# Kernel tuning notes

Hardware: AMD Instinct MI355X
Metric: run time of the kernel (lower is better)

The kernel has to match this reference:

```python
import jax, jax.numpy as jnp
import numpy as np

N = 50000      # nodes
E = 1600000    # edges (before self loops)
B = 512        # graphs
D = 128        # gcn dim (constant across the 3 GAT layers)
H = 1024       # hidden_dim
O = 128        # output_dim
NEG_SLOPE = 0.2


def setup_inputs() -> dict:
    key = jax.random.key(0)
    ks = jax.random.split(key, 24)
    inp = {
        "x": jax.random.normal(ks[0], (N, D), jnp.float32),
        "edge_index": jax.random.randint(ks[1], (2, E), 0, N, dtype=jnp.int64),
        "edge_weight": jax.random.uniform(ks[2], (E,), jnp.float32),
        "batch": jnp.sort(jax.random.randint(ks[3], (N,), 0, B, dtype=jnp.int64)),
    }
    s = 1.0 / np.sqrt(D)
    for i in range(3):
        k = 4 + 4 * i
        inp[f"W{i+1}"] = jax.random.normal(ks[k], (D, D), jnp.float32) * s
        inp[f"as{i+1}"] = jax.random.normal(ks[k + 1], (D,), jnp.float32) * s
        inp[f"ad{i+1}"] = jax.random.normal(ks[k + 2], (D,), jnp.float32) * s
        inp[f"b{i+1}"] = jnp.zeros((D,), jnp.float32)
    inp["Wf1"] = jax.random.normal(ks[16], (D, H), jnp.float32) * s
    inp["bf1"] = jnp.zeros((H,), jnp.float32)
    inp["Wf2"] = jax.random.normal(ks[17], (H, O), jnp.float32) * (1.0 / np.sqrt(H))
    inp["bf2"] = jnp.zeros((O,), jnp.float32)
    return inp


def gat_conv(x, src, dst, W, a_src, a_dst, b):
    """PyG GATConv, heads=1: gather -> leakyrelu -> segment softmax -> scatter-add."""
    h = x @ W                                   # [N, D]
    e = jax.nn.leaky_relu(jnp.take(h @ a_src, src) + jnp.take(h @ a_dst, dst), NEG_SLOPE)  # [E']
    m = jax.ops.segment_max(e, dst, num_segments=N)
    ex = jnp.exp(e - m[dst])
    denom = jax.ops.segment_sum(ex, dst, num_segments=N)
    alpha = ex / denom[dst]                      # segment softmax over incoming edges
    out = jax.ops.segment_sum(alpha[:, None] * h[src], dst, num_segments=N)
    return out + b


def reference(x, edge_index, edge_weight, batch,
              W1, as1, ad1, b1, W2, as2, ad2, b2, W3, as3, ad3, b3,
              Wf1, bf1, Wf2, bf2):
    # GATConv adds self loops; edge_weight is unused by GATConv (faithful to original)
    loop = jnp.arange(N, dtype=edge_index.dtype)
    src = jnp.concatenate([edge_index[0], loop])
    dst = jnp.concatenate([edge_index[1], loop])

    h = gat_conv(x, src, dst, W1, as1, ad1, b1)
    h = jax.nn.relu(gat_conv(h, src, dst, W2, as2, ad2, b2))
    h = jax.nn.relu(gat_conv(h, src, dst, W3, as3, ad3, b3))

    # global mean pool (gep)
    sums = jax.ops.segment_sum(h, batch, num_segments=B)        # [B, D]
    counts = jax.ops.segment_sum(jnp.ones((N,), h.dtype), batch, num_segments=B)
    pooled = sums / jnp.maximum(counts, 1.0)[:, None]

    # MLP head; dropout is identity at inference
    o = jax.nn.relu(pooled) @ Wf1 + bf1
    o = jax.nn.relu(o) @ Wf2 + bf2
    return o
```

## Files before the change

### kernel.cpp

```cpp
#include <hip/hip_runtime.h>
#include <cstdint>
#include <cstddef>

#define NEG_SLOPE 0.2f

typedef _Float16 f16x8 __attribute__((ext_vector_type(8)));
typedef float f32x4v __attribute__((ext_vector_type(4)));

__device__ __forceinline__ unsigned enc_f(float f) {
  unsigned u = __float_as_uint(f);
  return (u & 0x80000000u) ? ~u : (u | 0x80000000u);
}
__device__ __forceinline__ float dec_f(unsigned u) {
  return (u & 0x80000000u) ? __uint_as_float(u ^ 0x80000000u) : __uint_as_float(~u);
}

#define AST 136
#define ABYTES (64 * AST * 2)
#define SMEM_BYTES (ABYTES + 4 * 64 * 2 * 4)

__global__ void k_bounds_prep(const int* __restrict__ batch, int N, int B,
                              int* __restrict__ gstart, unsigned* __restrict__ maxPart,
                              int* __restrict__ counts,
                              const float* __restrict__ W1, const float* __restrict__ W2,
                              const float* __restrict__ W3,
                              _Float16* __restrict__ Wt1, _Float16* __restrict__ Wt2,
                              _Float16* __restrict__ Wt3, int nbb) {
  int b = blockIdx.x;
  if (b >= nbb) {
    int wi = b - nbb;
    const float* W = (wi == 0) ? W1 : (wi == 1) ? W2 : W3;
    _Float16* Wt = (wi == 0) ? Wt1 : (wi == 1) ? Wt2 : Wt3;
    for (int i = threadIdx.x; i < 2048; i += 256) {
      int k = i >> 4, n8 = (i & 15) << 3;
      float4 v0 = *(const float4*)&W[(size_t)k * 128 + n8];
      float4 v1 = *(const float4*)&W[(size_t)k * 128 + n8 + 4];
      Wt[(size_t)(n8 + 0) * 128 + k] = (_Float16)v0.x;
      Wt[(size_t)(n8 + 1) * 128 + k] = (_Float16)v0.y;
      Wt[(size_t)(n8 + 2) * 128 + k] = (_Float16)v0.z;
      Wt[(size_t)(n8 + 3) * 128 + k] = (_Float16)v0.w;
      Wt[(size_t)(n8 + 4) * 128 + k] = (_Float16)v1.x;
      Wt[(size_t)(n8 + 5) * 128 + k] = (_Float16)v1.y;
      Wt[(size_t)(n8 + 6) * 128 + k] = (_Float16)v1.z;
      Wt[(size_t)(n8 + 7) * 128 + k] = (_Float16)v1.w;
    }
    return;
  }
  int n = b * blockDim.x + threadIdx.x;
  if (n < 768) maxPart[n] = 0u;
  if (n >= N) return;
  counts[n] = 0;
  int cur = batch[n];
  if (n == 0) {
    for (int g = 0; g <= cur; g++) gstart[g] = 0;
  } else {
    int prev = batch[n - 1];
    for (int g = prev + 1; g <= cur; g++) gstart[g] = n;
  }
  if (n == N - 1) {
    for (int g = cur + 1; g <= B; g++) gstart[g] = N;
  }
}

__global__ void k_count_rank(const int* __restrict__ dst, int e0, int e1,
                             int* counts, int* __restrict__ rank) {
  int e = e0 + blockIdx.x * blockDim.x + threadIdx.x;
  if (e < e1) rank[e] = atomicAdd(&counts[dst[e]], 1);
}

__global__ __launch_bounds__(1024) void k_scan1(const int* __restrict__ counts, int N,
                                                int* __restrict__ row_ptr, int* __restrict__ part) {
  __shared__ int tmp[1024];
  int t = threadIdx.x;
  int i = blockIdx.x * 1024 + t;
  int v = (i < N) ? 1 + counts[i] : 0;
  tmp[t] = v;
  __syncthreads();
  for (int off = 1; off < 1024; off <<= 1) {
    int u = (t >= off) ? tmp[t - off] : 0;
    __syncthreads();
    tmp[t] += u;
    __syncthreads();
  }
  if (i < N) row_ptr[i + 1] = tmp[t];
  if (t == 1023) part[blockIdx.x] = tmp[t];
}

__global__ __launch_bounds__(1024) void k_scan3(int* __restrict__ row_ptr,
                                                const int* __restrict__ part, int N) {
  __shared__ int s_off;
  int bi = blockIdx.x;
  if (threadIdx.x == 0) {
    int run = 0;
    for (int b = 0; b < bi; b++) run += part[b];
    s_off = run;
    if (bi == 0) row_ptr[0] = 0;
  }
  __syncthreads();
  int i = bi * 1024 + threadIdx.x;
  if (i < N) row_ptr[i + 1] += s_off;
}

__device__ __forceinline__ void gemm_body(char* smem, int bx,
                                          const float* __restrict__ A32,
                                          const unsigned short* __restrict__ A16,
                                          const _Float16* __restrict__ WtG,
                                          unsigned short* __restrict__ hb,
                                          const float* __restrict__ asrc,
                                          const float* __restrict__ adst,
                                          float* __restrict__ sv, float* __restrict__ dv,
                                          unsigned* __restrict__ maxSlot, int M) {
  _Float16* Ah = (_Float16*)smem;
  float (*sred)[64][2] = (float (*)[64][2])(smem + ABYTES);
  int t = threadIdx.x;
  int rowbase = bx * 64;

  if (A16) {
    for (int i = t; i < 64 * 16; i += 256) {
      int r = i >> 4, c8 = (i & 15) << 3;
      int gr = rowbase + r;
      uint4 v = make_uint4(0u, 0u, 0u, 0u);
      if (gr < M) v = *(const uint4*)&A16[(size_t)gr * 128 + c8];
      *(uint4*)&Ah[r * AST + c8] = v;
    }
  } else {
    for (int i = t; i < 64 * 32; i += 256) {
      int r = i >> 5, c4 = (i & 31) << 2;
      int gr = rowbase + r;
      float4 v = make_float4(0.f, 0.f, 0.f, 0.f);
      if (gr < M) v = *(const float4*)&A32[(size_t)gr * 128 + c4];
      _Float16 tmp[4] = {(_Float16)v.x, (_Float16)v.y, (_Float16)v.z, (_Float16)v.w};
      *(short4*)&Ah[r * AST + c4] = *(short4*)tmp;
    }
  }
  __syncthreads();

  int wave = t >> 6, lane = t & 63, quad = lane >> 4, l15 = lane & 15;
  f32x4v acc[4][2];
#pragma unroll
  for (int mt = 0; mt < 4; mt++)
#pragma unroll
    for (int nt = 0; nt < 2; nt++) {
      acc[mt][nt][0] = 0.f; acc[mt][nt][1] = 0.f; acc[mt][nt][2] = 0.f; acc[mt][nt][3] = 0.f;
    }

#pragma unroll
  for (int s = 0; s < 4; s++) {
    int k0 = (s << 5) + (quad << 3);
    f16x8 af[4], bf[2];
#pragma unroll
    for (int mt = 0; mt < 4; mt++)
      af[mt] = *(f16x8*)&Ah[(mt * 16 + l15) * AST + k0];
#pragma unroll
    for (int nt = 0; nt < 2; nt++)
      bf[nt] = *(const f16x8*)&WtG[(size_t)(wave * 32 + nt * 16 + l15) * 128 + k0];
#pragma unroll
    for (int mt = 0; mt < 4; mt++)
#pragma unroll
      for (int nt = 0; nt < 2; nt++)
        acc[mt][nt] = __builtin_amdgcn_mfma_f32_16x16x32_f16(af[mt], bf[nt], acc[mt][nt], 0, 0, 0);
  }
  __syncthreads();

  float avv0 = asrc[wave * 32 + l15],      avv1 = asrc[wave * 32 + 16 + l15];
  float adv0 = adst[wave * 32 + l15],      adv1 = adst[wave * 32 + 16 + l15];
  _Float16* hS16 = (_Float16*)smem;
#pragma unroll
  for (int mt = 0; mt < 4; mt++) {
#pragma unroll
    for (int rr = 0; rr < 4; rr++) {
      int row = mt * 16 + quad * 4 + rr;
      hS16[row * AST + wave * 32 + l15]      = (_Float16)acc[mt][0][rr];
      hS16[row * AST + wave * 32 + 16 + l15] = (_Float16)acc[mt][1][rr];
      float ps = acc[mt][0][rr] * avv0 + acc[mt][1][rr] * avv1;
      float pd = acc[mt][0][rr] * adv0 + acc[mt][1][rr] * adv1;
#pragma unroll
      for (int mask = 8; mask; mask >>= 1) {
        ps += __shfl_xor(ps, mask);
        pd += __shfl_xor(pd, mask);
      }
      if (l15 == 0) { sred[wave][row][0] = ps; sred[wave][row][1] = pd; }
    }
  }
  __syncthreads();

  int tx = t & 31, ty = t >> 5;
#pragma unroll
  for (int r8 = 0; r8 < 8; r8++) {
    int row = r8 * 8 + ty;
    int gr = rowbase + row;
    if (gr < M)
      *(uint2*)&hb[(size_t)gr * 128 + tx * 4] = *(const uint2*)&hS16[row * AST + tx * 4];
  }

  if (t < 64) {
    int gr = rowbase + t;
    float ps = sred[0][t][0] + sred[1][t][0] + sred[2][t][0] + sred[3][t][0];
    float pd = sred[0][t][1] + sred[1][t][1] + sred[2][t][1] + sred[3][t][1];
    float wmax = -1e30f;
    if (gr < M) { sv[gr] = ps; dv[gr] = pd; wmax = ps; }
#pragma unroll
    for (int mask = 32; mask; mask >>= 1) wmax = fmaxf(wmax, __shfl_xor(wmax, mask));
    if (t == 0) atomicMax(&maxSlot[bx & 255], enc_f(wmax));
  }
}

__global__ __launch_bounds__(256) void k_fill_gemm(const int* __restrict__ src,
                                                   const int* __restrict__ dst,
                                                   const int* __restrict__ rank, int E, int N,
                                                   const int* __restrict__ row_ptr,
                                                   int* __restrict__ col,
                                                   const float* __restrict__ A32,
                                                   const _Float16* __restrict__ WtG,
                                                   unsigned short* __restrict__ hb,
                                                   const float* __restrict__ asrc,
                                                   const float* __restrict__ adst,
                                                   float* __restrict__ sv, float* __restrict__ dv,
                                                   unsigned* __restrict__ maxSlot, int Gg) {
  __shared__ __align__(16) char smem[SMEM_BYTES];
  int b = (int)blockIdx.x;
  bool isGemm = ((b % 9) == 4) && ((b / 9) < Gg);
  if (isGemm) {
    gemm_body(smem, b / 9, A32, (const unsigned short*)nullptr, WtG,
              hb, asrc, adst, sv, dv, maxSlot, N);
  } else {
    int nGemmBefore = (b >= 4) ? min((b - 4) / 9 + 1, Gg) : 0;
    int i = (b - nGemmBefore) * 256 + threadIdx.x;
    if (i < N) col[row_ptr[i]] = i;
    int e = i - N;
    if (e >= 0 && e < E) col[row_ptr[dst[e]] + 1 + rank[e]] = src[e];
  }
}

__global__ __launch_bounds__(256) void k_gemm_fused(const unsigned short* __restrict__ A16,
                                                    const _Float16* __restrict__ WtG,
                                                    unsigned short* __restrict__ hb,
                                                    const float* __restrict__ asrc,
                                                    const float* __restrict__ adst,
                                                    float* __restrict__ sv, float* __restrict__ dv,
                                                    unsigned* __restrict__ maxSlot, int M) {
  __shared__ __align__(16) char smem[SMEM_BYTES];
  gemm_body(smem, (int)blockIdx.x, (const float*)nullptr, A16, WtG,
            hb, asrc, adst, sv, dv, maxSlot, M);
}

__global__ __launch_bounds__(256) void k_agg(const unsigned short* __restrict__ hb,
                                             const float* __restrict__ sv,
                                             const float* __restrict__ dv,
                                             const int* __restrict__ row_ptr,
                                             const int* __restrict__ col,
                                             const float* __restrict__ bias,
                                             const unsigned* __restrict__ maxSlot,
                                             unsigned short* __restrict__ out16,
                                             int N, int relu) {
  int wid = (int)((blockIdx.x * (size_t)blockDim.x + threadIdx.x) >> 6);
  int lane = threadIdx.x & 63;
  if (wid >= N) return;

  unsigned mp = max(max(maxSlot[lane], maxSlot[lane + 64]),
                    max(maxSlot[lane + 128], maxSlot[lane + 192]));
#pragma unroll
  for (int off = 32; off; off >>= 1) mp = max(mp, __shfl_xor(mp, off));
  float maxS = dec_f(mp);

  int beg = row_ptr[wid], end = row_ptr[wid + 1];
  float dn = dv[wid];
  float m = maxS + dn;
  m = (m > 0.f) ? m : NEG_SLOPE * m;

  int g = lane >> 4, sub = lane & 15;
  const uint32_t* hbu = (const uint32_t*)hb;
  float acc[8];
#pragma unroll
  for (int k = 0; k < 8; k++) acc[k] = 0.f;
  float dsum = 0.f;

#define FETCH_SLOT(K, W, H)                                                \
  {                                                                        \
    int sl = ((K) << 2) + g;                                               \
    int sn = __shfl(sn_l, sl);                                             \
    W = __shfl(w_l, sl);                                                   \
    H = make_uint4(0u, 0u, 0u, 0u);                                        \
    if (sl < cnt) H = *(const uint4*)(hbu + (size_t)sn * 64 + sub * 4);    \
  }
#define ACC_SLOT(W, H)                                                     \
  {                                                                        \
    const _Float16* hp = (const _Float16*)&H;                              \
    _Pragma("unroll")                                                      \
    for (int q = 0; q < 8; q++) acc[q] += W * (float)hp[q];                \
  }

  for (int base = beg; base < end; base += 64) {
    int cnt = min(end - base, 64);

    int sn_l = 0;
    float w_l = 0.f;
    if (lane < cnt) {
      sn_l = col[base + lane];
      float e = sv[sn_l] + dn;
      e = (e > 0.f) ? e : NEG_SLOPE * e;
      w_l = __expf(e - m);
      dsum += w_l;
    }

    int kmaxW = (cnt + 3) >> 2;
    float wA, wB, wC, wD, wE, wF;
    uint4 hA, hB, hC, hD, hE, hF;
    FETCH_SLOT(0, wA, hA);
    FETCH_SLOT(1, wB, hB);
    FETCH_SLOT(2, wC, hC);
    FETCH_SLOT(3, wD, hD);
    FETCH_SLOT(4, wE, hE);
    for (int k = 5; k < kmaxW; k++) {
      FETCH_SLOT(k, wF, hF);
      ACC_SLOT(wA, hA);
      wA = wB; hA = hB;
      wB = wC; hB = hC;
      wC = wD; hC = hD;
      wD = wE; hD = hE;
      wE = wF; hE = hF;
    }
    ACC_SLOT(wA, hA);
    ACC_SLOT(wB, hB);
    ACC_SLOT(wC, hC);
    ACC_SLOT(wD, hD);
    ACC_SLOT(wE, hE);
  }

#pragma unroll
  for (int off = 1; off < 64; off <<= 1) dsum += __shfl_xor(dsum, off);
#pragma unroll
  for (int k = 0; k < 8; k++) {
    acc[k] += __shfl_xor(acc[k], 16);
    acc[k] += __shfl_xor(acc[k], 32);
  }
  if (lane < 16) {
    float inv = 1.f / dsum;
    float o[8];
    const float* bp = &bias[sub * 8];
#pragma unroll
    for (int k = 0; k < 8; k++) {
      o[k] = acc[k] * inv + bp[k];
      if (relu) o[k] = fmaxf(o[k], 0.f);
    }
    _Float16 q[8];
#pragma unroll
    for (int k = 0; k < 8; k++) q[k] = (_Float16)o[k];
    *(uint4*)&out16[(size_t)wid * 128 + sub * 8] = *(uint4*)q;
  }
}

__global__ __launch_bounds__(256) void k_pool(const unsigned short* __restrict__ h16,
                                              const int* __restrict__ gstart,
                                              float* __restrict__ pooled, int B) {
  __shared__ float red[4][128];
  int b = blockIdx.x, t = threadIdx.x;
  int c = t & 63, seg = t >> 6;
  int s0 = gstart[b], s1 = gstart[b + 1];
  int cnt = s1 - s0;
  int per = (cnt + 3) >> 2;
  int n0 = s0 + seg * per;
  int n1 = min(n0 + per, s1);
  const uint32_t* hu = (const uint32_t*)h16;
  float a0 = 0.f, a1 = 0.f;
  for (int n = n0; n < n1; n++) {
    union { uint32_t u; _Float16 h[2]; } cv;
    cv.u = hu[(size_t)n * 64 + c];
    a0 += (float)cv.h[0];
    a1 += (float)cv.h[1];
  }
  if (seg) { red[seg][2 * c] = a0; red[seg][2 * c + 1] = a1; }
  __syncthreads();
  if (seg == 0) {
    a0 += red[1][2 * c] + red[2][2 * c] + red[3][2 * c];
    a1 += red[1][2 * c + 1] + red[2][2 * c + 1] + red[3][2 * c + 1];
    float inv = 1.f / (float)(cnt > 0 ? cnt : 1);
    pooled[b * 128 + 2 * c]     = fmaxf(a0 * inv, 0.f);
    pooled[b * 128 + 2 * c + 1] = fmaxf(a1 * inv, 0.f);
  }
}

__global__ __launch_bounds__(256) void k_mlp(const float* __restrict__ pooled,
                                             const float* __restrict__ Wf1,
                                             const float* __restrict__ bf1,
                                             const float* __restrict__ Wf2,
                                             const float* __restrict__ bf2,
                                             float* __restrict__ out, int B) {
  __shared__ float P[4][128];
  __shared__ float H1[4][1024];
  __shared__ float R[4][128];
  int t = threadIdx.x;
  int g0 = blockIdx.x * 4;

  for (int i = t; i < 4 * 128; i += 256) {
    int gi = i >> 7, c = i & 127;
    P[gi][c] = (g0 + gi < B) ? pooled[(size_t)(g0 + gi) * 128 + c] : 0.f;
  }
  __syncthreads();

#pragma unroll
  for (int cb = 0; cb < 4; cb++) {
    int c = cb * 256 + t;
    float a0 = 0.f, a1 = 0.f, a2 = 0.f, a3 = 0.f;
    for (int k = 0; k < 128; k++) {
      float w = Wf1[(size_t)k * 1024 + c];
      a0 += P[0][k] * w; a1 += P[1][k] * w; a2 += P[2][k] * w; a3 += P[3][k] * w;
    }
    float b = bf1[c];
    H1[0][c] = fmaxf(a0 + b, 0.f);
    H1[1][c] = fmaxf(a1 + b, 0.f);
    H1[2][c] = fmaxf(a2 + b, 0.f);
    H1[3][c] = fmaxf(a3 + b, 0.f);
  }
  __syncthreads();

  int c = t & 127, hh = t >> 7;
  float a0 = 0.f, a1 = 0.f, a2 = 0.f, a3 = 0.f;
  int k0 = hh * 512;
  for (int k = k0; k < k0 + 512; k++) {
    float w = Wf2[(size_t)k * 128 + c];
    a0 += H1[0][k] * w; a1 += H1[1][k] * w; a2 += H1[2][k] * w; a3 += H1[3][k] * w;
  }
  if (hh == 1) { R[0][c] = a0; R[1][c] = a1; R[2][c] = a2; R[3][c] = a3; }
  __syncthreads();
  if (hh == 0) {
    float b = bf2[c];
    float o0 = a0 + R[0][c] + b;
    float o1 = a1 + R[1][c] + b;
    float o2 = a2 + R[2][c] + b;
    float o3 = a3 + R[3][c] + b;
    if (g0 + 0 < B) out[(size_t)(g0 + 0) * 128 + c] = o0;
    if (g0 + 1 < B) out[(size_t)(g0 + 1) * 128 + c] = o1;
    if (g0 + 2 < B) out[(size_t)(g0 + 2) * 128 + c] = o2;
    if (g0 + 3 < B) out[(size_t)(g0 + 3) * 128 + c] = o3;
  }
}

extern "C" void kernel_launch(void* const* d_in, const int* in_sizes, int n_in,
                              void* d_out, int out_size, void* d_ws, size_t ws_size,
                              hipStream_t stream) {
  const float* x     = (const float*)d_in[0];
  const int*   ei    = (const int*)d_in[1];
  const int*   batch = (const int*)d_in[3];
  const float* W1 = (const float*)d_in[4];
  const float* as1 = (const float*)d_in[5];
  const float* ad1 = (const float*)d_in[6];
  const float* b1 = (const float*)d_in[7];
  const float* W2 = (const float*)d_in[8];
  const float* as2 = (const float*)d_in[9];
  const float* ad2 = (const float*)d_in[10];
  const float* b2 = (const float*)d_in[11];
  const float* W3 = (const float*)d_in[12];
  const float* as3 = (const float*)d_in[13];
  const float* ad3 = (const float*)d_in[14];
  const float* b3 = (const float*)d_in[15];
  const float* Wf1 = (const float*)d_in[16];
  const float* bf1 = (const float*)d_in[17];
  const float* Wf2 = (const float*)d_in[18];
  const float* bf2 = (const float*)d_in[19];

  const int N = in_sizes[0] / 128;
  const int E = in_sizes[1] / 2;
  const int B = out_size / 128;

  char* base_ws = (char*)d_ws;
  size_t off = 0;
  auto carve = [&](size_t bytes) -> void* {
    off = (off + 255) & ~(size_t)255;
    void* p = base_ws + off;
    off += bytes;
    return p;
  };
  int* counts   = (int*)carve((size_t)N * 4);
  int* row_ptr  = (int*)carve((size_t)(N + 1) * 4);
  int* rank     = (int*)carve((size_t)E * 4);
  int* col      = (int*)carve((size_t)(E + N) * 4);
  int* part     = (int*)carve(1024 * 4);
  int* gstart   = (int*)carve((size_t)(B + 1) * 4);
  unsigned* maxPart = (unsigned*)carve(768 * 4);
  float* sbuf   = (float*)carve((size_t)N * 4);
  float* dbuf   = (float*)carve((size_t)N * 4);
  unsigned short* hb  = (unsigned short*)carve((size_t)N * 128 * 2);
  unsigned short* a16 = (unsigned short*)carve((size_t)N * 128 * 2);
  float* pooled = (float*)carve((size_t)B * 128 * 4);
  _Float16* Wt1 = (_Float16*)carve(128 * 128 * 2);
  _Float16* Wt2 = (_Float16*)carve(128 * 128 * 2);
  _Float16* Wt3 = (_Float16*)carve(128 * 128 * 2);

  const int* srcp = ei;
  const int* dstp = ei + E;
  const int nb = (N + 1023) / 1024;
  const int Gg = (N + 63) / 64;
  const int Gf = (E + N + 255) / 256;
  const int nbb = (N + 255) / 256;
  const int Eh = E / 2;

  hipLaunchKernelGGL(k_bounds_prep, dim3(nbb + 3), dim3(256), 0, stream,
                     batch, N, B, gstart, maxPart, counts,
                     W1, W2, W3, Wt1, Wt2, Wt3, nbb);
  hipLaunchKernelGGL(k_count_rank, dim3((Eh + 255) / 256), dim3(256), 0, stream,
                     dstp, 0, Eh, counts, rank);
  hipLaunchKernelGGL(k_count_rank, dim3((E - Eh + 255) / 256), dim3(256), 0, stream,
                     dstp, Eh, E, counts, rank);
  hipLaunchKernelGGL(k_scan1, dim3(nb), dim3(1024), 0, stream, counts, N, row_ptr, part);
  hipLaunchKernelGGL(k_scan3, dim3(nb), dim3(1024), 0, stream, row_ptr, part, N);

  hipLaunchKernelGGL(k_fill_gemm, dim3(Gf + Gg), dim3(256), 0, stream,
                     srcp, dstp, rank, E, N, row_ptr, col,
                     x, Wt1, hb, as1, ad1, sbuf, dbuf, maxPart + 0 * 256, Gg);

  hipLaunchKernelGGL(k_agg, dim3((N + 3) / 4), dim3(256), 0, stream,
                     hb, sbuf, dbuf, row_ptr, col, b1, maxPart + 0 * 256, a16, N, 0);

  hipLaunchKernelGGL(k_gemm_fused, dim3(Gg), dim3(256), 0, stream,
                     a16, Wt2, hb, as2, ad2, sbuf, dbuf, maxPart + 1 * 256, N);
  hipLaunchKernelGGL(k_agg, dim3((N + 3) / 4), dim3(256), 0, stream,
                     hb, sbuf, dbuf, row_ptr, col, b2, maxPart + 1 * 256, a16, N, 1);

  hipLaunchKernelGGL(k_gemm_fused, dim3(Gg), dim3(256), 0, stream,
                     a16, Wt3, hb, as3, ad3, sbuf, dbuf, maxPart + 2 * 256, N);
  hipLaunchKernelGGL(k_agg, dim3((N + 3) / 4), dim3(256), 0, stream,
                     hb, sbuf, dbuf, row_ptr, col, b3, maxPart + 2 * 256, a16, N, 1);

  hipLaunchKernelGGL(k_pool, dim3(B), dim3(256), 0, stream, a16, gstart, pooled, B);
  hipLaunchKernelGGL(k_mlp, dim3((B + 3) / 4), dim3(256), 0, stream,
                     pooled, Wf1, bf1, Wf2, bf2, (float*)d_out, B);
}
```

Before: 524.7 us.

## Run MLP head on MFMA with fp16 transposed weights and unroll agg pipeline

Replaces the scalar fp32 MLP kernel with two MFMA-based kernels (k_mlp1 for the 128x1024 layer, k_mlp2 for the 1024x128 layer). They use fp16 pooled activations and fp16 transposed copies of Wf1/Wf2 built in the prep kernel. The aggregation loop's register-rotation pipeline is also unrolled by six to remove the per-iteration register moves. This trades some precision (fp16 pooled/hidden activations) and an extra launch for far fewer ALU cycles in the MLP head. The mlp2 kernel uses only 8 blocks, so it has low parallelism.

```diff
diff --git a/kernel.cpp b/kernel.cpp
--- a/kernel.cpp
+++ b/kernel.cpp
@@ -24,25 +24,41 @@
                               int* __restrict__ counts,
                               const float* __restrict__ W1, const float* __restrict__ W2,
                               const float* __restrict__ W3,
+                              const float* __restrict__ Wf1, const float* __restrict__ Wf2,
                               _Float16* __restrict__ Wt1, _Float16* __restrict__ Wt2,
-                              _Float16* __restrict__ Wt3, int nbb) {
+                              _Float16* __restrict__ Wt3,
+                              _Float16* __restrict__ Wf1t, _Float16* __restrict__ Wf2t,
+                              int nbb) {
   int b = blockIdx.x;
   if (b >= nbb) {
-    int wi = b - nbb;
-    const float* W = (wi == 0) ? W1 : (wi == 1) ? W2 : W3;
-    _Float16* Wt = (wi == 0) ? Wt1 : (wi == 1) ? Wt2 : Wt3;
+    int ti = b - nbb;
+    const float* src;
+    _Float16* dst;
+    int lds_, ldd_, k0, n0;
+    if (ti < 3) {
+      src = (ti == 0) ? W1 : (ti == 1) ? W2 : W3;
+      dst = (ti == 0) ? Wt1 : (ti == 1) ? Wt2 : Wt3;
+      lds_ = 128; ldd_ = 128; k0 = 0; n0 = 0;
+    } else if (ti < 11) {
+      int j = ti - 3;
+      src = Wf1; dst = Wf1t; lds_ = 1024; ldd_ = 128; k0 = 0; n0 = j * 128;
+    } else {
+      int j = ti - 11;
+      src = Wf2; dst = Wf2t; lds_ = 128; ldd_ = 1024; k0 = j * 128; n0 = 0;
+    }
     for (int i = threadIdx.x; i < 2048; i += 256) {
       int k = i >> 4, n8 = (i & 15) << 3;
-      float4 v0 = *(const float4*)&W[(size_t)k * 128 + n8];
-      float4 v1 = *(const float4*)&W[(size_t)k * 128 + n8 + 4];
-      Wt[(size_t)(n8 + 0) * 128 + k] = (_Float16)v0.x;
-      Wt[(size_t)(n8 + 1) * 128 + k] = (_Float16)v0.y;
-      Wt[(size_t)(n8 + 2) * 128 + k] = (_Float16)v0.z;
-      Wt[(size_t)(n8 + 3) * 128 + k] = (_Float16)v0.w;
-      Wt[(size_t)(n8 + 4) * 128 + k] = (_Float16)v1.x;
-      Wt[(size_t)(n8 + 5) * 128 + k] = (_Float16)v1.y;
-      Wt[(size_t)(n8 + 6) * 128 + k] = (_Float16)v1.z;
-      Wt[(size_t)(n8 + 7) * 128 + k] = (_Float16)v1.w;
+      const float* s = &src[(size_t)(k0 + k) * lds_ + n0 + n8];
+      float4 v0 = *(const float4*)&s[0];
+      float4 v1 = *(const float4*)&s[4];
+      dst[(size_t)(n0 + n8 + 0) * ldd_ + k0 + k] = (_Float16)v0.x;
+      dst[(size_t)(n0 + n8 + 1) * ldd_ + k0 + k] = (_Float16)v0.y;
+      dst[(size_t)(n0 + n8 + 2) * ldd_ + k0 + k] = (_Float16)v0.z;
+      dst[(size_t)(n0 + n8 + 3) * ldd_ + k0 + k] = (_Float16)v0.w;
+      dst[(size_t)(n0 + n8 + 4) * ldd_ + k0 + k] = (_Float16)v1.x;
+      dst[(size_t)(n0 + n8 + 5) * ldd_ + k0 + k] = (_Float16)v1.y;
+      dst[(size_t)(n0 + n8 + 6) * ldd_ + k0 + k] = (_Float16)v1.z;
+      dst[(size_t)(n0 + n8 + 7) * ldd_ + k0 + k] = (_Float16)v1.w;
     }
     return;
   }
@@ -311,9 +327,17 @@
     FETCH_SLOT(2, wC, hC);
     FETCH_SLOT(3, wD, hD);
     FETCH_SLOT(4, wE, hE);
-    for (int k = 5; k < kmaxW; k++) {
-      FETCH_SLOT(k, wF, hF);
-      ACC_SLOT(wA, hA);
+    int k = 5;
+    for (; k + 5 < kmaxW; k += 6) {
+      FETCH_SLOT(k + 0, wF, hF); ACC_SLOT(wA, hA);
+      FETCH_SLOT(k + 1, wA, hA); ACC_SLOT(wB, hB);
+      FETCH_SLOT(k + 2, wB, hB); ACC_SLOT(wC, hC);
+      FETCH_SLOT(k + 3, wC, hC); ACC_SLOT(wD, hD);
+      FETCH_SLOT(k + 4, wD, hD); ACC_SLOT(wE, hE);
+      FETCH_SLOT(k + 5, wE, hE); ACC_SLOT(wF, hF);
+    }
+    for (; k < kmaxW; k++) {
+      FETCH_SLOT(k, wF, hF); ACC_SLOT(wA, hA);
       wA = wB; hA = hB;
       wB = wC; hB = hC;
       wC = wD; hC = hD;
@@ -352,7 +376,7 @@
 
 __global__ __launch_bounds__(256) void k_pool(const unsigned short* __restrict__ h16,
                                               const int* __restrict__ gstart,
-                                              float* __restrict__ pooled, int B) {
+                                              unsigned short* __restrict__ pooled16, int B) {
   __shared__ float red[4][128];
   int b = blockIdx.x, t = threadIdx.x;
   int c = t & 63, seg = t >> 6;
@@ -375,65 +399,130 @@
     a0 += red[1][2 * c] + red[2][2 * c] + red[3][2 * c];
     a1 += red[1][2 * c + 1] + red[2][2 * c + 1] + red[3][2 * c + 1];
     float inv = 1.f / (float)(cnt > 0 ? cnt : 1);
-    pooled[b * 128 + 2 * c]     = fmaxf(a0 * inv, 0.f);
-    pooled[b * 128 + 2 * c + 1] = fmaxf(a1 * inv, 0.f);
-  }
-}
-
-__global__ __launch_bounds__(256) void k_mlp(const float* __restrict__ pooled,
-                                             const float* __restrict__ Wf1,
-                                             const float* __restrict__ bf1,
-                                             const float* __restrict__ Wf2,
-                                             const float* __restrict__ bf2,
-                                             float* __restrict__ out, int B) {
-  __shared__ float P[4][128];
-  __shared__ float H1[4][1024];
-  __shared__ float R[4][128];
+    union { uint32_t u; _Float16 h[2]; } ov;
+    ov.h[0] = (_Float16)fmaxf(a0 * inv, 0.f);
+    ov.h[1] = (_Float16)fmaxf(a1 * inv, 0.f);
+    *(uint32_t*)&pooled16[(size_t)b * 128 + 2 * c] = ov.u;
+  }
+}
+
+__global__ __launch_bounds__(256) void k_mlp1(const unsigned short* __restrict__ P16,
+                                              const _Float16* __restrict__ Wf1t,
+                                              const float* __restrict__ bf1,
+                                              unsigned short* __restrict__ H1g, int B, int nRow) {
+  __shared__ __align__(16) _Float16 Ah[64 * AST];
+  int bx = (int)blockIdx.x;
+  int rowt = bx % nRow, colt = bx / nRow;
+  int rowbase = rowt * 64;
   int t = threadIdx.x;
-  int g0 = blockIdx.x * 4;
-
-  for (int i = t; i < 4 * 128; i += 256) {
-    int gi = i >> 7, c = i & 127;
-    P[gi][c] = (g0 + gi < B) ? pooled[(size_t)(g0 + gi) * 128 + c] : 0.f;
+
+  for (int i = t; i < 64 * 16; i += 256) {
+    int r = i >> 4, c8 = (i & 15) << 3;
+    int gr = rowbase + r;
+    uint4 v = make_uint4(0u, 0u, 0u, 0u);
+    if (gr < B) v = *(const uint4*)&P16[(size_t)gr * 128 + c8];
+    *(uint4*)&Ah[r * AST + c8] = v;
   }
   __syncthreads();
 
-#pragma unroll
-  for (int cb = 0; cb < 4; cb++) {
-    int c = cb * 256 + t;
-    float a0 = 0.f, a1 = 0.f, a2 = 0.f, a3 = 0.f;
-    for (int k = 0; k < 128; k++) {
-      float w = Wf1[(size_t)k * 1024 + c];
-      a0 += P[0][k] * w; a1 += P[1][k] * w; a2 += P[2][k] * w; a3 += P[3][k] * w;
-    }
-    float b = bf1[c];
-    H1[0][c] = fmaxf(a0 + b, 0.f);
-    H1[1][c] = fmaxf(a1 + b, 0.f);
-    H1[2][c] = fmaxf(a2 + b, 0.f);
-    H1[3][c] = fmaxf(a3 + b, 0.f);
-  }
-  __syncthreads();
-
-  int c = t & 127, hh = t >> 7;
-  float a0 = 0.f, a1 = 0.f, a2 = 0.f, a3 = 0.f;
-  int k0 = hh * 512;
-  for (int k = k0; k < k0 + 512; k++) {
-    float w = Wf2[(size_t)k * 128 + c];
-    a0 += H1[0][k] * w; a1 += H1[1][k] * w; a2 += H1[2][k] * w; a3 += H1[3][k] * w;
-  }
-  if (hh == 1) { R[0][c] = a0; R[1][c] = a1; R[2][c] = a2; R[3][c] = a3; }
-  __syncthreads();
-  if (hh == 0) {
-    float b = bf2[c];
-    float o0 = a0 + R[0][c] + b;
-    float o1 = a1 + R[1][c] + b;
-    float o2 = a2 + R[2][c] + b;
-    float o3 = a3 + R[3][c] + b;
-    if (g0 + 0 < B) out[(size_t)(g0 + 0) * 128 + c] = o0;
-    if (g0 + 1 < B) out[(size_t)(g0 + 1) * 128 + c] = o1;
-    if (g0 + 2 < B) out[(size_t)(g0 + 2) * 128 + c] = o2;
-    if (g0 + 3 < B) out[(size_t)(g0 + 3) * 128 + c] = o3;
-  }
+  int wave = t >> 6, lane = t & 63, quad = lane >> 4, l15 = lane & 15;
+  int colbase = colt * 128 + wave * 32;
+  f32x4v acc[4][2];
+#pragma unroll
+  for (int mt = 0; mt < 4; mt++)
+#pragma unroll
+    for (int nt = 0; nt < 2; nt++) {
+      acc[mt][nt][0] = 0.f; acc[mt][nt][1] = 0.f; acc[mt][nt][2] = 0.f; acc[mt][nt][3] = 0.f;
+    }
+#pragma unroll
+  for (int s = 0; s < 4; s++) {
+    int k0 = (s << 5) + (quad << 3);
+    f16x8 af[4], bf[2];
+#pragma unroll
+    for (int mt = 0; mt < 4; mt++)
+      af[mt] = *(f16x8*)&Ah[(mt * 16 + l15) * AST + k0];
+#pragma unroll
+    for (int nt = 0; nt < 2; nt++)
+      bf[nt] = *(const f16x8*)&Wf1t[(size_t)(colbase + nt * 16 + l15) * 128 + k0];
+#pragma unroll
+    for (int mt = 0; mt < 4; mt++)
+#pragma unroll
+      for (int nt = 0; nt < 2; nt++)
+        acc[mt][nt] = __builtin_amdgcn_mfma_f32_16x16x32_f16(af[mt], bf[nt], acc[mt][nt], 0, 0, 0);
+  }
+
+  float b0 = bf1[colbase + l15], b1 = bf1[colbase + 16 + l15];
+#pragma unroll
+  for (int mt = 0; mt < 4; mt++)
+#pragma unroll
+    for (int rr = 0; rr < 4; rr++) {
+      int gr = rowbase + mt * 16 + quad * 4 + rr;
+      if (gr < B) {
+        H1g[(size_t)gr * 1024 + colbase + l15] =
+            (unsigned short)__builtin_bit_cast(unsigned short, (_Float16)fmaxf(acc[mt][0][rr] + b0, 0.f));
+        H1g[(size_t)gr * 1024 + colbase + 16 + l15] =
+            (unsigned short)__builtin_bit_cast(unsigned short, (_Float16)fmaxf(acc[mt][1][rr] + b1, 0.f));
+      }
+    }
+}
+
+__global__ __launch_bounds__(256) void k_mlp2(const unsigned short* __restrict__ H1g,
+                                              const _Float16* __restrict__ Wf2t,
+                                              const float* __restrict__ bf2,
+                                              float* __restrict__ out, int B) {
+  __shared__ __align__(16) _Float16 Ah[64 * AST];
+  int rowbase = (int)blockIdx.x * 64;
+  int t = threadIdx.x;
+  int wave = t >> 6, lane = t & 63, quad = lane >> 4, l15 = lane & 15;
+
+  f32x4v acc[4][2];
+#pragma unroll
+  for (int mt = 0; mt < 4; mt++)
+#pragma unroll
+    for (int nt = 0; nt < 2; nt++) {
+      acc[mt][nt][0] = 0.f; acc[mt][nt][1] = 0.f; acc[mt][nt][2] = 0.f; acc[mt][nt][3] = 0.f;
+    }
+
+  for (int kc = 0; kc < 8; kc++) {
+    for (int i = t; i < 64 * 16; i += 256) {
+      int r = i >> 4, c8 = (i & 15) << 3;
+      int gr = rowbase + r;
+      uint4 v = make_uint4(0u, 0u, 0u, 0u);
+      if (gr < B) v = *(const uint4*)&H1g[(size_t)gr * 1024 + kc * 128 + c8];
+      *(uint4*)&Ah[r * AST + c8] = v;
+    }
+    __syncthreads();
+#pragma unroll
+    for (int s = 0; s < 4; s++) {
+      int k0 = (s << 5) + (quad << 3);
+      f16x8 af[4], bf[2];
+#pragma unroll
+      for (int mt = 0; mt < 4; mt++)
+        af[mt] = *(f16x8*)&Ah[(mt * 16 + l15) * AST + k0];
+#pragma unroll
+      for (int nt = 0; nt < 2; nt++)
+        bf[nt] = *(const f16x8*)&Wf2t[(size_t)(wave * 32 + nt * 16 + l15) * 1024 + kc * 128 + k0];
+#pragma unroll
+      for (int mt = 0; mt < 4; mt++)
+#pragma unroll
+        for (int nt = 0; nt < 2; nt++)
+          acc[mt][nt] = __builtin_amdgcn_mfma_f32_16x16x32_f16(af[mt], bf[nt], acc[mt][nt], 0, 0, 0);
+    }
+    __syncthreads();
+  }
+
+  int col0 = wave * 32 + l15, col1 = col0 + 16;
+  float b0 = bf2[col0], b1 = bf2[col1];
+#pragma unroll
+  for (int mt = 0; mt < 4; mt++)
+#pragma unroll
+    for (int rr = 0; rr < 4; rr++) {
+      int gr = rowbase + mt * 16 + quad * 4 + rr;
+      if (gr < B) {
+        out[(size_t)gr * 128 + col0] = acc[mt][0][rr] + b0;
+        out[(size_t)gr * 128 + col1] = acc[mt][1][rr] + b1;
+      }
+    }
 }
 
 extern "C" void kernel_launch(void* const* d_in, const int* in_sizes, int n_in,
@@ -482,10 +571,13 @@
   float* dbuf   = (float*)carve((size_t)N * 4);
   unsigned short* hb  = (unsigned short*)carve((size_t)N * 128 * 2);
   unsigned short* a16 = (unsigned short*)carve((size_t)N * 128 * 2);
-  float* pooled = (float*)carve((size_t)B * 128 * 4);
+  unsigned short* pooled16 = (unsigned short*)carve((size_t)B * 128 * 2);
+  unsigned short* H1g = (unsigned short*)carve((size_t)B * 1024 * 2);
   _Float16* Wt1 = (_Float16*)carve(128 * 128 * 2);
   _Float16* Wt2 = (_Float16*)carve(128 * 128 * 2);
   _Float16* Wt3 = (_Float16*)carve(128 * 128 * 2);
+  _Float16* Wf1t = (_Float16*)carve((size_t)1024 * 128 * 2);
+  _Float16* Wf2t = (_Float16*)carve((size_t)128 * 1024 * 2);
 
   const int* srcp = ei;
   const int* dstp = ei + E;
@@ -493,11 +585,12 @@
   const int Gg = (N + 63) / 64;
   const int Gf = (E + N + 255) / 256;
   const int nbb = (N + 255) / 256;
+  const int nRow = (B + 63) / 64;
   const int Eh = E / 2;
 
-  hipLaunchKernelGGL(k_bounds_prep, dim3(nbb + 3), dim3(256), 0, stream,
+  hipLaunchKernelGGL(k_bounds_prep, dim3(nbb + 19), dim3(256), 0, stream,
                      batch, N, B, gstart, maxPart, counts,
-                     W1, W2, W3, Wt1, Wt2, Wt3, nbb);
+                     W1, W2, W3, Wf1, Wf2, Wt1, Wt2, Wt3, Wf1t, Wf2t, nbb);
   hipLaunchKernelGGL(k_count_rank, dim3((Eh + 255) / 256), dim3(256), 0, stream,
                      dstp, 0, Eh, counts, rank);
   hipLaunchKernelGGL(k_count_rank, dim3((E - Eh + 255) / 256), dim3(256), 0, stream,
@@ -522,7 +615,9 @@
   hipLaunchKernelGGL(k_agg, dim3((N + 3) / 4), dim3(256), 0, stream,
                      hb, sbuf, dbuf, row_ptr, col, b3, maxPart + 2 * 256, a16, N, 1);
 
-  hipLaunchKernelGGL(k_pool, dim3(B), dim3(256), 0, stream, a16, gstart, pooled, B);
-  hipLaunchKernelGGL(k_mlp, dim3((B + 3) / 4), dim3(256), 0, stream,
-                     pooled, Wf1, bf1, Wf2, bf2, (float*)d_out, B);
-}
+  hipLaunchKernelGGL(k_pool, dim3(B), dim3(256), 0, stream, a16, gstart, pooled16, B);
+  hipLaunchKernelGGL(k_mlp1, dim3(nRow * 8), dim3(256), 0, stream,
+                     pooled16, Wf1t, bf1, H1g, B, nRow);
+  hipLaunchKernelGGL(k_mlp2, dim3(nRow), dim3(256), 0, stream,
+                     H1g, Wf2t, bf2, (float*)d_out, B);
+}
```

New measurement: 591.9 us. +12.8%, slower.
